# Optimization experiments

Hardware: AMD Instinct MI355X
Metric: run time of the kernel (lower is better)

The kernel has to match this reference:

```python
import jax, jax.numpy as jnp
import numpy as np

MASK_FILL = -987654321.0


def rotate_every_two(x):
    # pairs (x0, x1) -> (-x1, x0), interleaved back along last dim
    x1 = x[..., 0::2]
    x2 = x[..., 1::2]
    return jnp.stack((-x2, x1), axis=-1).reshape(x.shape)


def setup_inputs() -> dict:
    key = jax.random.key(0)
    ks = jax.random.split(key, 6)
    b, n, dim = 64, 197, 768
    heads, dim_head = 12, 64
    inner = heads * dim_head
    x = jax.random.normal(ks[0], (b, n, dim), dtype=jnp.float32)
    pos_emb = jax.random.normal(ks[1], (1, n, dim_head), dtype=jnp.float32)
    w_qkv = jax.random.normal(ks[2], (dim, 3 * inner), dtype=jnp.float32) * (dim ** -0.5)
    scale = jnp.full((heads,), dim_head ** -0.5, dtype=jnp.float32)
    w_out = jax.random.normal(ks[3], (inner, dim), dtype=jnp.float32) * (inner ** -0.5)
    b_out = jnp.zeros((dim,), dtype=jnp.float32)
    return {"x": x, "pos_emb": pos_emb, "w_qkv": w_qkv, "scale": scale,
            "w_out": w_out, "b_out": b_out}


def reference(x, pos_emb, w_qkv, scale, w_out, b_out):
    b, n, dim = x.shape
    h = scale.shape[0]
    qkv = x @ w_qkv                         # [b, n, 3*inner]
    q, k, v = jnp.split(qkv, 3, axis=-1)
    dh = q.shape[-1] // h
    to_heads = lambda t: t.reshape(b, n, h, dh).transpose(0, 2, 1, 3)  # bhnd
    q, k, v = to_heads(q), to_heads(k), to_heads(v)

    # RoPE: pos_emb [1, n, (2 * dh/2)] -> sin/cos [n, dh/2] -> interleave to [n, dh]
    sc = pos_emb[0].reshape(n, 2, dh // 2)
    sin = jnp.repeat(sc[:, 0], 2, axis=-1)  # [n, dh]
    cos = jnp.repeat(sc[:, 1], 2, axis=-1)
    q = q * cos + rotate_every_two(q) * sin
    k = k * cos + rotate_every_two(k) * sin

    # per-head learnable scale
    dots = jnp.einsum('bhid,bhjd->bhij', q, k) * scale[None, :, None, None]
    # diagonal (LSA) mask
    eye = jnp.eye(n, dtype=bool)
    dots = jnp.where(eye, MASK_FILL, dots)

    attn = jax.nn.softmax(dots, axis=-1)
    out = jnp.einsum('bhij,bhjd->bhid', attn, v)
    out = out.transpose(0, 2, 1, 3).reshape(b, n, h * dh)
    return out @ w_out + b_out
```

## Files before the change

### kernel.cpp

```cpp
#include <hip/hip_runtime.h>
#include <math.h>

#define MASK_FILL_F (-987654321.0f)

typedef unsigned short u16;
typedef unsigned int   u32;

constexpr int Bb   = 64;
constexpr int Ntok = 197;
constexpr int Dim  = 768;
constexpr int Heads= 12;
constexpr int Dh   = 64;
constexpr int Nq3  = 2304;
constexpr int Rows = 12608;
constexpr int Mpad = 12672;

using f32x4  = __attribute__((ext_vector_type(4))) float;
using bf16x8 = __attribute__((ext_vector_type(8))) short;

__device__ __forceinline__ u16 f2bf(float f) {
  u32 u = __float_as_uint(f);
  u = (u + 0x7fffu + ((u >> 16) & 1u)) >> 16;
  return (u16)u;
}

__device__ __forceinline__ void stage16(const void* gp, void* lp) {
  __builtin_amdgcn_global_load_lds(
      (const __attribute__((address_space(1))) u32*)gp,
      (__attribute__((address_space(3))) u32*)lp, 16, 0, 0);
}

__device__ __forceinline__ int sigma6(int M) {
  return (M & 0x23) | (((M >> 3) & 1) << 4) | (((M >> 2) & 1) << 3) |
         (((M >> 4) & 1) << 2);
}

__global__ __launch_bounds__(256) void cvt_bf16(const float* __restrict__ in,
                                                u16* __restrict__ out, int n4) {
  const int i = blockIdx.x * 256 + threadIdx.x;
  if (i < n4) {
    const float4 v = *(const float4*)&in[(size_t)i * 4];
    ushort4 u;
    u.x = f2bf(v.x); u.y = f2bf(v.y); u.z = f2bf(v.z); u.w = f2bf(v.w);
    *(ushort4*)&out[(size_t)i * 4] = u;
  }
}

__global__ __launch_bounds__(256) void transpose_cvt(const float* __restrict__ in,
                                                     u16* __restrict__ out,
                                                     int R, int C) {
  __shared__ float t[32][33];
  const int c0 = blockIdx.x * 32, r0 = blockIdx.y * 32;
  const int tx = threadIdx.x & 31, ty = threadIdx.x >> 5;
#pragma unroll
  for (int rr = ty; rr < 32; rr += 8)
    t[rr][tx] = in[(size_t)(r0 + rr) * C + c0 + tx];
  __syncthreads();
#pragma unroll
  for (int cc = ty; cc < 32; cc += 8)
    out[(size_t)(c0 + cc) * R + r0 + tx] = f2bf(t[tx][cc]);
}

__global__ __launch_bounds__(256) void vtrans(const u16* __restrict__ qkvB,
                                              u16* __restrict__ vT) {
  __shared__ u16 t[64 * 72];
  const int jt = blockIdx.x, bh = blockIdx.y;
  const int b = bh / Heads, h = bh % Heads;
  const int j0 = jt * 64;
  const int tid = threadIdx.x;

  for (int idx = tid; idx < 512; idx += 256) {
    const int jr = idx >> 3, c8 = (idx & 7) * 8;
    const int j = j0 + jr;
    uint4 u = make_uint4(0u, 0u, 0u, 0u);
    if (j < Ntok)
      u = *(const uint4*)(qkvB + (size_t)(b * Ntok + j) * Nq3 + 2 * Dim + h * Dh + c8);
    *(uint4*)&t[jr * 72 + c8] = u;
  }
  __syncthreads();
  for (int idx = tid; idx < 512; idx += 256) {
    const int d = idx >> 3, j8 = (idx & 7) * 8;
    ushort4 lo, hi;
    lo.x = t[(j8 + 0) * 72 + d]; lo.y = t[(j8 + 1) * 72 + d];
    lo.z = t[(j8 + 2) * 72 + d]; lo.w = t[(j8 + 3) * 72 + d];
    hi.x = t[(j8 + 4) * 72 + d]; hi.y = t[(j8 + 5) * 72 + d];
    hi.z = t[(j8 + 6) * 72 + d]; hi.w = t[(j8 + 7) * 72 + d];
    u16* dst = vT + ((size_t)bh * 64 + d) * 256 + j0 + j8;
    *(ushort4*)dst       = lo;
    *(ushort4*)(dst + 4) = hi;
  }
}

constexpr int Kc  = 768;
constexpr int NKT = Kc / 64;

#define BARM() asm volatile("s_barrier" ::: "memory")
#define VMW4() asm volatile("s_waitcnt vmcnt(4)" ::: "memory")
#define VMW2() asm volatile("s_waitcnt vmcnt(2)" ::: "memory")
#define VMW0() asm volatile("s_waitcnt vmcnt(0)" ::: "memory")

#define PH(MH, NH, RDA, RDB, STG, ...)                                         \
  do {                                                                         \
    if (RDA) {                                                                 \
      _Pragma("unroll") for (int m_ = 0; m_ < 4; ++m_)                         \
      _Pragma("unroll") for (int k_ = 0; k_ < 2; ++k_)                         \
        af[m_][k_] = *(const bf16x8*)&Asb[((MH) * 64 + mrow + m_ * 16) * 64    \
                                          + (((k_ * 4 + qd) ^ sx) * 8)];       \
    }                                                                          \
    if (RDB) {                                                                 \
      _Pragma("unroll") for (int n_ = 0; n_ < 2; ++n_)                         \
      _Pragma("unroll") for (int k_ = 0; k_ < 2; ++k_)                         \
        bfr[n_][k_] = *(const bf16x8*)&Bsb[((NH) * 32 + nrow + n_ * 16) * 64   \
                                           + (((k_ * 4 + qd) ^ sx) * 8)];      \
    }                                                                          \
    STG;                                                                       \
    BARM();                                                                    \
    __builtin_amdgcn_s_setprio(1);                                             \
    _Pragma("unroll") for (int m_ = 0; m_ < 4; ++m_)                           \
    _Pragma("unroll") for (int n_ = 0; n_ < 2; ++n_)                           \
    _Pragma("unroll") for (int k_ = 0; k_ < 2; ++k_)                           \
      acc[(MH) * 4 + m_][(NH) * 2 + n_] =                                      \
          __builtin_amdgcn_mfma_f32_16x16x32_bf16(                             \
              af[m_][k_], bfr[n_][k_],                                         \
              acc[(MH) * 4 + m_][(NH) * 2 + n_], 0, 0, 0);                     \
    __builtin_amdgcn_s_setprio(0);                                             \
    __VA_ARGS__;                                                               \
    BARM();                                                                    \
  } while (0)

template<int MODE, int TN>
__global__ __launch_bounds__(512, 2) void gemm8p(
    const u16* __restrict__ Ag, const u16* __restrict__ Bg,
    void* __restrict__ Cv, int Nn, int nwg,
    const float* __restrict__ pe, const float* __restrict__ bias)
{
  __shared__ u16 As[2][256 * 64];
  __shared__ u16 Bs[2][256 * 64];

  const int tid = threadIdx.x, lane = tid & 63, w = tid >> 6;

  const int orig = blockIdx.x;
  const int q8 = nwg >> 3, r8 = nwg & 7;
  const int xcd = orig & 7, sub = orig >> 3;
  const int wgid = (xcd < r8 ? xcd * (q8 + 1) : r8 * (q8 + 1) + (xcd - r8) * q8) + sub;
  const int tm = wgid / TN, tn = wgid % TN;
  const int m0 = tm * 256, n0 = tn * 256;

  const int wr = w >> 2, wc = w & 3;
  const int tx = lane & 15, qd = lane >> 4, sx = tx & 7;
  const int mrow = wr * 128 + tx, nrow = wc * 64 + tx;

  const int srow = lane >> 3;
  const int scol = ((lane & 7) ^ srow) * 8;
  const int a1c = (w & 1) * 16 + (w >> 1) * 2, a2c = a1c + 1;
  const int a3c = a1c + 8,                     a4c = a2c + 8;
  const int b1c = (w & 3) * 8 + (w >> 2) * 2,  b2c = b1c + 1;
  const int b3c = b1c + 4,                     b4c = b2c + 4;

  const u16* sA1 = Ag + (size_t)(m0 + 8 * a1c + srow) * Kc + scol;
  const u16* sA2 = Ag + (size_t)(m0 + 8 * a2c + srow) * Kc + scol;
  const u16* sA3 = Ag + (size_t)(m0 + 8 * a3c + srow) * Kc + scol;
  const u16* sA4 = Ag + (size_t)(m0 + 8 * a4c + srow) * Kc + scol;
  const u16* sB1 = Bg + (size_t)(n0 + 8 * b1c + srow) * Kc + scol;
  const u16* sB2 = Bg + (size_t)(n0 + 8 * b2c + srow) * Kc + scol;
  const u16* sB3 = Bg + (size_t)(n0 + 8 * b3c + srow) * Kc + scol;
  const u16* sB4 = Bg + (size_t)(n0 + 8 * b4c + srow) * Kc + scol;

  stage16(sA1, &As[0][a1c * 512]); stage16(sB1, &Bs[0][b1c * 512]);
  stage16(sA2, &As[0][a2c * 512]); stage16(sB2, &Bs[0][b2c * 512]);
  stage16(sB3, &Bs[0][b3c * 512]); stage16(sB4, &Bs[0][b4c * 512]);
  stage16(sA3, &As[0][a3c * 512]); stage16(sA4, &As[0][a4c * 512]);
  sA1 += 64; sA2 += 64; sA3 += 64; sA4 += 64;
  sB1 += 64; sB2 += 64; sB3 += 64; sB4 += 64;
  VMW4();
  BARM();

  f32x4  acc[8][4] = {};
  bf16x8 af[4][2], bfr[2][2];

  int cur = 0;
#pragma unroll 1
  for (int t = 0; t < NKT - 1; ++t) {
    const u16* Asb = As[cur];
    const u16* Bsb = Bs[cur];
    u16* An = As[cur ^ 1];
    u16* Bn = Bs[cur ^ 1];

    PH(0, 0, 1, 1,
       { stage16(sA1, &An[a1c * 512]); stage16(sB1, &Bn[b1c * 512]); }, VMW4());
    PH(0, 1, 0, 1,
       { stage16(sA2, &An[a2c * 512]); stage16(sB2, &Bn[b2c * 512]); }, VMW4());
    PH(1, 1, 1, 0,
       { stage16(sB3, &Bn[b3c * 512]); stage16(sB4, &Bn[b4c * 512]); }, );
    PH(1, 0, 0, 1,
       { stage16(sA3, &An[a3c * 512]); stage16(sA4, &An[a4c * 512]); }, VMW4());

    sA1 += 64; sA2 += 64; sA3 += 64; sA4 += 64;
    sB1 += 64; sB2 += 64; sB3 += 64; sB4 += 64;
    cur ^= 1;
  }
  {
    const u16* Asb = As[cur];
    const u16* Bsb = Bs[cur];
    PH(0, 0, 1, 1, {}, VMW2());
    PH(0, 1, 0, 1, {}, VMW0());
    PH(1, 1, 1, 0, {}, );
    PH(1, 0, 0, 1, {}, );
  }

  if (MODE == 0) {
    u16* C = (u16*)Cv;
    const bool dorot = (n0 < 2 * Dim);
#pragma unroll
    for (int mi = 0; mi < 8; ++mi) {
      const int rbase = m0 + wr * 128 + mi * 16 + qd * 4;
      int iq[4];
#pragma unroll
      for (int r = 0; r < 4; ++r) iq[r] = (rbase + r) % Ntok;
#pragma unroll
      for (int ni = 0; ni < 4; ++ni) {
        const int col = n0 + wc * 64 + ni * 16 + tx;
        const int mm  = (col & 63) >> 1;
        const int odd = col & 1;
#pragma unroll
        for (int r = 0; r < 4; ++r) {
          float v = acc[mi][ni][r];
          float res = v;
          if (dorot) {
            const float other = __shfl_xor(v, 1, 64);
            const float sn = pe[iq[r] * 64 + mm];
            const float c2 = pe[iq[r] * 64 + 32 + mm];
            res = odd ? (v * c2 + other * sn) : (v * c2 - other * sn);
          }
          C[(size_t)(rbase + r) * Nn + col] = f2bf(res);
        }
      }
    }
  } else {
    float* C = (float*)Cv;
#pragma unroll
    for (int mi = 0; mi < 8; ++mi) {
      const int rbase = m0 + wr * 128 + mi * 16 + qd * 4;
#pragma unroll
      for (int ni = 0; ni < 4; ++ni) {
        const int col = n0 + wc * 64 + ni * 16 + tx;
        const float bv = bias[col];
#pragma unroll
        for (int r = 0; r < 4; ++r) {
          const int row = rbase + r;
          if (row < Rows) C[(size_t)row * Nn + col] = acc[mi][ni][r] + bv;
        }
      }
    }
  }
}

constexpr int LS = 72;

__global__ __launch_bounds__(256) void attn7(
    const u16* __restrict__ qkvB, const u16* __restrict__ vT,
    const float* __restrict__ scale, u16* __restrict__ outB)
{
  __shared__ u16 ks [64 * LS];
  __shared__ u16 vts[64 * LS];

  const int it = blockIdx.x, bh = blockIdx.y;
  const int b = bh / Heads, h = bh % Heads;
  const int i0 = it * 128;
  const float sc = scale[h];
  const int tid = threadIdx.x, lane = tid & 63, w = tid >> 6;
  const int tx = lane & 15, q = lane >> 4;
  const size_t rowbase = (size_t)b * Ntok;

  bf16x8 bq[2][2];
#pragma unroll
  for (int g = 0; g < 2; ++g)
#pragma unroll
    for (int kk = 0; kk < 2; ++kk)
      bq[g][kk] = *(const bf16x8*)(qkvB +
          (rowbase + i0 + 32 * w + 16 * g + tx) * (size_t)Nq3 + h * Dh + kk * 32 + q * 8);

  float l_part[2] = {0.f, 0.f};
  f32x4 oacc[2][4] = {};

  for (int jt = 0; jt < 4; ++jt) {
    const int j0 = jt * 64;
    __syncthreads();

    for (int idx = tid; idx < 512; idx += 256) {
      const int M = idx >> 3, c8 = (idx & 7) * 8;
      const int js = sigma6(M);
      *(uint4*)&ks[M * LS + c8] =
          *(const uint4*)(qkvB + (rowbase + j0 + js) * (size_t)Nq3 + Dim + h * Dh + c8);
    }
    for (int idx = tid; idx < 512; idx += 256) {
      const int d = idx >> 3, c8 = (idx & 7) * 8;
      *(uint4*)&vts[d * LS + c8] =
          *(const uint4*)(vT + ((size_t)bh * 64 + d) * 256 + j0 + c8);
    }
    __syncthreads();

#pragma unroll
    for (int g = 0; g < 2; ++g) {
      f32x4 sT[4] = {};
#pragma unroll
      for (int kk = 0; kk < 2; ++kk)
#pragma unroll
        for (int jb = 0; jb < 4; ++jb) {
          const bf16x8 ka = *(const bf16x8*)&ks[(jb * 16 + tx) * LS + kk * 32 + q * 8];
          sT[jb] = __builtin_amdgcn_mfma_f32_16x16x32_bf16(ka, bq[g][kk], sT[jb], 0, 0, 0);
        }

      const int ig = i0 + 32 * w + 16 * g + tx;
      union { bf16x8 v; u16 e[8]; } pk[2];
      float lp = 0.f;
#pragma unroll
      for (int jb = 0; jb < 4; ++jb)
#pragma unroll
        for (int r = 0; r < 4; ++r) {
          const int jg = j0 + 32 * (jb >> 1) + 8 * q + 4 * (jb & 1) + r;
          const float s = fminf(sT[jb][r] * sc, 80.f);
          const bool bad = (jg >= Ntok) || (jg == ig);
          const float p = bad ? 0.f : __expf(s);
          lp += p;
          pk[jb >> 1].e[(jb & 1) * 4 + r] = f2bf(p);
        }
      l_part[g] += lp;

#pragma unroll
      for (int kk = 0; kk < 2; ++kk)
#pragma unroll
        for (int nb = 0; nb < 4; ++nb) {
          const bf16x8 vb = *(const bf16x8*)&vts[(nb * 16 + tx) * LS + kk * 32 + q * 8];
          oacc[g][nb] = __builtin_amdgcn_mfma_f32_16x16x32_bf16(pk[kk].v, vb,
                                                               oacc[g][nb], 0, 0, 0);
        }
    }
  }

#pragma unroll
  for (int g = 0; g < 2; ++g) {
    float l = l_part[g];
    l += __shfl_xor(l, 16, 64);
    l += __shfl_xor(l, 32, 64);
    const float linv = 1.0f / l;
#pragma unroll
    for (int r = 0; r < 4; ++r) {
      const float lr = __shfl(linv, 4 * q + r, 64);
      const int igr = i0 + 32 * w + 16 * g + 4 * q + r;
      if (igr < Ntok) {
#pragma unroll
        for (int nb = 0; nb < 4; ++nb)
          outB[(rowbase + igr) * (size_t)Dim + h * Dh + nb * 16 + tx] =
              f2bf(oacc[g][nb][r] * lr);
      }
    }
  }
}

extern "C" void kernel_launch(void* const* d_in, const int* in_sizes, int n_in,
                              void* d_out, int out_size, void* d_ws, size_t ws_size,
                              hipStream_t stream) {
  const float* x     = (const float*)d_in[0];
  const float* pe    = (const float*)d_in[1];
  const float* w_qkv = (const float*)d_in[2];
  const float* scale = (const float*)d_in[3];
  const float* w_out = (const float*)d_in[4];
  const float* b_out = (const float*)d_in[5];
  float* out = (float*)d_out;

  u16* xb    = (u16*)d_ws;
  u16* wqkvT = xb    + (size_t)Mpad * Dim;
  u16* woutT = wqkvT + (size_t)Nq3 * Dim;
  u16* qkvB  = woutT + (size_t)Dim * Dim;
  u16* attnB = qkvB  + (size_t)Mpad * Nq3;
  u16* vT    = attnB + (size_t)Mpad * Dim;

  cvt_bf16<<<(Rows * Dim / 4 + 255) / 256, 256, 0, stream>>>(x, xb, Rows * Dim / 4);
  transpose_cvt<<<dim3(Nq3 / 32, Dim / 32), 256, 0, stream>>>(w_qkv, wqkvT, Dim, Nq3);
  transpose_cvt<<<dim3(Dim / 32, Dim / 32), 256, 0, stream>>>(w_out, woutT, Dim, Dim);

  constexpr int NWG0 = 50 * 9;
  gemm8p<0, 9><<<NWG0, 512, 0, stream>>>(xb, wqkvT, qkvB, Nq3, NWG0, pe, nullptr);

  vtrans<<<dim3(4, Bb * Heads), 256, 0, stream>>>(qkvB, vT);

  attn7<<<dim3(2, Bb * Heads), 256, 0, stream>>>(qkvB, vT, scale, attnB);

  constexpr int NWG1 = 50 * 3;
  gemm8p<1, 3><<<NWG1, 512, 0, stream>>>(attnB, woutT, out, Dim, NWG1, nullptr, b_out);
}
```

Measured before the change: 284.1 us.

## Restructure GEMM main loop into unrolled two-tile pipeline with interleaved partial-buffer staging

```diff
diff --git a/kernel.cpp b/kernel.cpp
--- a/kernel.cpp
+++ b/kernel.cpp
@@ -96,37 +96,33 @@
 
 #define BARM() asm volatile("s_barrier" ::: "memory")
 #define VMW4() asm volatile("s_waitcnt vmcnt(4)" ::: "memory")
-#define VMW2() asm volatile("s_waitcnt vmcnt(2)" ::: "memory")
-#define VMW0() asm volatile("s_waitcnt vmcnt(0)" ::: "memory")
-
-#define PH(MH, NH, RDA, RDB, STG, ...)                                         \
-  do {                                                                         \
-    if (RDA) {                                                                 \
-      _Pragma("unroll") for (int m_ = 0; m_ < 4; ++m_)                         \
-      _Pragma("unroll") for (int k_ = 0; k_ < 2; ++k_)                         \
-        af[m_][k_] = *(const bf16x8*)&Asb[((MH) * 64 + mrow + m_ * 16) * 64    \
-                                          + (((k_ * 4 + qd) ^ sx) * 8)];       \
-    }                                                                          \
-    if (RDB) {                                                                 \
-      _Pragma("unroll") for (int n_ = 0; n_ < 2; ++n_)                         \
-      _Pragma("unroll") for (int k_ = 0; k_ < 2; ++k_)                         \
-        bfr[n_][k_] = *(const bf16x8*)&Bsb[((NH) * 32 + nrow + n_ * 16) * 64   \
-                                           + (((k_ * 4 + qd) ^ sx) * 8)];      \
-    }                                                                          \
-    STG;                                                                       \
-    BARM();                                                                    \
-    __builtin_amdgcn_s_setprio(1);                                             \
-    _Pragma("unroll") for (int m_ = 0; m_ < 4; ++m_)                           \
-    _Pragma("unroll") for (int n_ = 0; n_ < 2; ++n_)                           \
-    _Pragma("unroll") for (int k_ = 0; k_ < 2; ++k_)                           \
-      acc[(MH) * 4 + m_][(NH) * 2 + n_] =                                      \
-          __builtin_amdgcn_mfma_f32_16x16x32_bf16(                             \
-              af[m_][k_], bfr[n_][k_],                                         \
-              acc[(MH) * 4 + m_][(NH) * 2 + n_], 0, 0, 0);                     \
-    __builtin_amdgcn_s_setprio(0);                                             \
-    __VA_ARGS__;                                                               \
-    BARM();                                                                    \
-  } while (0)
+
+#define STGA(chunk, kt, BUF) \
+  stage16(Ag + (size_t)(m0 + (chunk) * 8 + srow) * Kc + (kt) * 64 + scol, \
+          &As[BUF][(chunk) * 512])
+#define STGB(chunk, kt, BUF) \
+  stage16(Bg + (size_t)(n0 + (chunk) * 8 + srow) * Kc + (kt) * 64 + scol, \
+          &Bs[BUF][(chunk) * 512])
+
+#define RDA(BUF, MH) \
+  _Pragma("unroll") for (int m_ = 0; m_ < 4; ++m_) \
+  _Pragma("unroll") for (int k_ = 0; k_ < 2; ++k_) \
+    af[m_][k_] = *(const bf16x8*)&As[BUF][(wr * 128 + (MH) * 64 + m_ * 16 + tx) * 64 \
+                                          + (((k_ * 4 + qd) ^ sx) * 8)];
+#define RDB(BUF, NH, BFR) \
+  _Pragma("unroll") for (int n_ = 0; n_ < 2; ++n_) \
+  _Pragma("unroll") for (int k_ = 0; k_ < 2; ++k_) \
+    BFR[n_][k_] = *(const bf16x8*)&Bs[BUF][(wc * 64 + (NH) * 32 + n_ * 16 + tx) * 64 \
+                                           + (((k_ * 4 + qd) ^ sx) * 8)];
+
+#define MM(MH, NH, BFR) \
+  __builtin_amdgcn_s_setprio(1); \
+  _Pragma("unroll") for (int m_ = 0; m_ < 4; ++m_) \
+  _Pragma("unroll") for (int n_ = 0; n_ < 2; ++n_) \
+  _Pragma("unroll") for (int k_ = 0; k_ < 2; ++k_) \
+    acc[(MH) * 4 + m_][(NH) * 2 + n_] = __builtin_amdgcn_mfma_f32_16x16x32_bf16( \
+        af[m_][k_], BFR[n_][k_], acc[(MH) * 4 + m_][(NH) * 2 + n_], 0, 0, 0); \
+  __builtin_amdgcn_s_setprio(0);
 
 template<int MODE, int TN>
 __global__ __launch_bounds__(512, 2) void gemm8p(
@@ -148,64 +144,48 @@
 
   const int wr = w >> 2, wc = w & 3;
   const int tx = lane & 15, qd = lane >> 4, sx = tx & 7;
-  const int mrow = wr * 128 + tx, nrow = wc * 64 + tx;
 
   const int srow = lane >> 3;
   const int scol = ((lane & 7) ^ srow) * 8;
-  const int a1c = (w & 1) * 16 + (w >> 1) * 2, a2c = a1c + 1;
-  const int a3c = a1c + 8,                     a4c = a2c + 8;
-  const int b1c = (w & 3) * 8 + (w >> 2) * 2,  b2c = b1c + 1;
-  const int b3c = b1c + 4,                     b4c = b2c + 4;
-
-  const u16* sA1 = Ag + (size_t)(m0 + 8 * a1c + srow) * Kc + scol;
-  const u16* sA2 = Ag + (size_t)(m0 + 8 * a2c + srow) * Kc + scol;
-  const u16* sA3 = Ag + (size_t)(m0 + 8 * a3c + srow) * Kc + scol;
-  const u16* sA4 = Ag + (size_t)(m0 + 8 * a4c + srow) * Kc + scol;
-  const u16* sB1 = Bg + (size_t)(n0 + 8 * b1c + srow) * Kc + scol;
-  const u16* sB2 = Bg + (size_t)(n0 + 8 * b2c + srow) * Kc + scol;
-  const u16* sB3 = Bg + (size_t)(n0 + 8 * b3c + srow) * Kc + scol;
-  const u16* sB4 = Bg + (size_t)(n0 + 8 * b4c + srow) * Kc + scol;
-
-  stage16(sA1, &As[0][a1c * 512]); stage16(sB1, &Bs[0][b1c * 512]);
-  stage16(sA2, &As[0][a2c * 512]); stage16(sB2, &Bs[0][b2c * 512]);
-  stage16(sB3, &Bs[0][b3c * 512]); stage16(sB4, &Bs[0][b4c * 512]);
-  stage16(sA3, &As[0][a3c * 512]); stage16(sA4, &As[0][a4c * 512]);
-  sA1 += 64; sA2 += 64; sA3 += 64; sA4 += 64;
-  sB1 += 64; sB2 += 64; sB3 += 64; sB4 += 64;
+  const int b0 = (w >> 1) * 8 + (w & 1) * 2;
+
+  STGA(w, 0, 0);        STGA(16 + w, 0, 0);
+  STGB(b0 + 4, 0, 0);   STGB(b0 + 5, 0, 0);
+  STGA(8 + w, 0, 0);    STGA(24 + w, 0, 0);
+  STGB(b0, 0, 0);       STGB(b0 + 1, 0, 0);
+  STGA(w, 1, 1);        STGA(16 + w, 1, 1);
+  STGB(b0 + 4, 1, 1);   STGB(b0 + 5, 1, 1);
   VMW4();
   BARM();
 
   f32x4  acc[8][4] = {};
-  bf16x8 af[4][2], bfr[2][2];
-
-  int cur = 0;
+  bf16x8 af[4][2], bf0[2][2], bf1[2][2];
+
 #pragma unroll 1
-  for (int t = 0; t < NKT - 1; ++t) {
-    const u16* Asb = As[cur];
-    const u16* Bsb = Bs[cur];
-    u16* An = As[cur ^ 1];
-    u16* Bn = Bs[cur ^ 1];
-
-    PH(0, 0, 1, 1,
-       { stage16(sA1, &An[a1c * 512]); stage16(sB1, &Bn[b1c * 512]); }, VMW4());
-    PH(0, 1, 0, 1,
-       { stage16(sA2, &An[a2c * 512]); stage16(sB2, &Bn[b2c * 512]); }, VMW4());
-    PH(1, 1, 1, 0,
-       { stage16(sB3, &Bn[b3c * 512]); stage16(sB4, &Bn[b4c * 512]); }, );
-    PH(1, 0, 0, 1,
-       { stage16(sA3, &An[a3c * 512]); stage16(sA4, &An[a4c * 512]); }, VMW4());
-
-    sA1 += 64; sA2 += 64; sA3 += 64; sA4 += 64;
-    sB1 += 64; sB2 += 64; sB3 += 64; sB4 += 64;
-    cur ^= 1;
-  }
-  {
-    const u16* Asb = As[cur];
-    const u16* Bsb = Bs[cur];
-    PH(0, 0, 1, 1, {}, VMW2());
-    PH(0, 1, 0, 1, {}, VMW0());
-    PH(1, 1, 1, 0, {}, );
-    PH(1, 0, 0, 1, {}, );
+  for (int i = 0; i < NKT / 2; ++i) {
+    const int u = 2 * i;
+    RDA(0, 0); RDB(0, 0, bf0);
+    STGA(8 + w, u + 1, 1); STGA(24 + w, u + 1, 1);
+    BARM(); MM(0, 0, bf0); BARM();
+    RDB(0, 1, bf1);
+    STGB(b0, u + 1, 1); STGB(b0 + 1, u + 1, 1);
+    BARM(); MM(0, 1, bf1); BARM();
+    RDA(0, 1);
+    STGA(w, u + 2, 0); STGA(16 + w, u + 2, 0);
+    BARM(); MM(1, 1, bf1); BARM();
+    STGB(b0 + 4, u + 2, 0); STGB(b0 + 5, u + 2, 0);
+    BARM(); MM(1, 0, bf0); VMW4(); BARM();
+    RDA(1, 0); RDB(1, 0, bf0);
+    STGA(8 + w, u + 2, 0); STGA(24 + w, u + 2, 0);
+    BARM(); MM(0, 0, bf0); BARM();
+    RDB(1, 1, bf1);
+    STGB(b0, u + 2, 0); STGB(b0 + 1, u + 2, 0);
+    BARM(); MM(0, 1, bf1); BARM();
+    RDA(1, 1);
+    STGA(w, u + 3, 1); STGA(16 + w, u + 3, 1);
+    BARM(); MM(1, 1, bf1); BARM();
+    STGB(b0 + 4, u + 3, 1); STGB(b0 + 5, u + 3, 1);
+    BARM(); MM(1, 0, bf0); VMW4(); BARM();
   }
 
   if (MODE == 0) {
```

New measurement: 282.9 us. No clear change (-0.4%).
